# Kernel optimization log

Hardware: AMD Instinct MI355X
Metric: run time of the kernel (lower is better)

The kernel has to match this reference:

```python
import jax, jax.numpy as jnp
import numpy as np

N_NODES = 50000
N_EDGES = 800000
IN_FEATS = 128
N_HIDDEN = 128
N_CLASSES = 64


def setup_inputs() -> dict:
    key = jax.random.key(0)
    ks = jax.random.split(key, 12)
    x = jax.random.normal(ks[0], (N_NODES, IN_FEATS), dtype=jnp.float32)
    src = jax.random.randint(ks[1], (N_EDGES,), 0, N_NODES, dtype=jnp.int32)
    dst = jax.random.randint(ks[2], (N_EDGES,), 0, N_NODES, dtype=jnp.int32)
    dims = [(IN_FEATS, N_HIDDEN), (N_HIDDEN, N_HIDDEN), (N_HIDDEN, N_CLASSES)]
    inp = {"x": x, "src": src, "dst": dst}
    for i, (din, dout) in enumerate(dims):
        s = (2.0 / (din + dout)) ** 0.5  # xavier-ish init scale
        inp[f"Wself{i}"] = jax.random.normal(ks[3 + 3 * i], (din, dout), dtype=jnp.float32) * s
        inp[f"Wneigh{i}"] = jax.random.normal(ks[4 + 3 * i], (din, dout), dtype=jnp.float32) * s
        inp[f"b{i}"] = jnp.zeros((dout,), dtype=jnp.float32)
    return inp


def _sage_conv(h, src, dst, inv_deg, Wself, Wneigh, b):
    # mean aggregation over in-neighbors: gather on src, segment-sum on dst
    agg = jax.ops.segment_sum(h[src], dst, num_segments=N_NODES)  # [N, d]
    h_neigh = agg * inv_deg[:, None]
    return h @ Wself + h_neigh @ Wneigh + b


def reference(x, src, dst, Wself0, Wneigh0, b0, Wself1, Wneigh1, b1, Wself2, Wneigh2, b2):
    # in-degree (clamped to 1, matching DGL mean aggregator), shared across layers
    deg = jax.ops.segment_sum(jnp.ones((N_EDGES,), dtype=jnp.float32), dst, num_segments=N_NODES)
    inv_deg = 1.0 / jnp.maximum(deg, 1.0)
    # dropout is identity in eval mode
    h = _sage_conv(x, src, dst, inv_deg, Wself0, Wneigh0, b0)
    h = jax.nn.relu(h)
    h = _sage_conv(h, src, dst, inv_deg, Wself1, Wneigh1, b1)
    h = jax.nn.relu(h)
    h = _sage_conv(h, src, dst, inv_deg, Wself2, Wneigh2, b2)
    return h
```

## Files before the change

kernel.cpp:

```cpp
#include <hip/hip_runtime.h>

#define N_NODES 50000
#define N_EDGES 800000
#define NB_SCAN 196

typedef unsigned short ushort_t;
typedef __attribute__((ext_vector_type(8))) short  short8v;
typedef __attribute__((ext_vector_type(4))) float  float4v;
typedef __attribute__((ext_vector_type(4))) unsigned short ushort4v;
typedef __attribute__((ext_vector_type(8))) unsigned short ushort8v;

__device__ __forceinline__ ushort_t f2bf(float f) {
    unsigned u = __float_as_uint(f);
    unsigned r = 0x7fffu + ((u >> 16) & 1u);
    return (ushort_t)((u + r) >> 16);
}
__device__ __forceinline__ float bf2f(ushort_t h) {
    return __uint_as_float((unsigned)h << 16);
}

__global__ __launch_bounds__(256) void cast_zero_k(const float* __restrict__ x,
                                                   ushort_t* __restrict__ xb,
                                                   int* __restrict__ deg, int n4) {
    int i = blockIdx.x * 256 + threadIdx.x;
    if (i < n4) {
        float4 v = ((const float4*)x)[i];
        ushort4v h;
        h[0] = f2bf(v.x); h[1] = f2bf(v.y); h[2] = f2bf(v.z); h[3] = f2bf(v.w);
        ((ushort4v*)xb)[i] = h;
    }
    if (i < N_NODES) deg[i] = 0;
}

__global__ __launch_bounds__(256) void deg_count_k(const int4* __restrict__ dst4,
                                                   int* __restrict__ deg) {
    const int grp = blockIdx.x & 7;
    const int lo = grp * 6250, hi = lo + 6250;
    const int stride = (gridDim.x >> 3) * 256;
    const int n4 = N_EDGES / 4;
    for (int i = (blockIdx.x >> 3) * 256 + threadIdx.x; i < n4; i += stride) {
        int4 d = dst4[i];
        if (d.x >= lo && d.x < hi) atomicAdd(deg + d.x, 1);
        if (d.y >= lo && d.y < hi) atomicAdd(deg + d.y, 1);
        if (d.z >= lo && d.z < hi) atomicAdd(deg + d.z, 1);
        if (d.w >= lo && d.w < hi) atomicAdd(deg + d.w, 1);
    }
}

__global__ __launch_bounds__(256) void block_sum_k(const int* __restrict__ deg,
                                                   int* __restrict__ bsum, int n) {
    __shared__ int s[256];
    int t = threadIdx.x, b = blockIdx.x;
    int i = b * 256 + t;
    s[t] = (i < n) ? deg[i] : 0;
    __syncthreads();
#pragma unroll
    for (int off = 128; off > 0; off >>= 1) {
        if (t < off) s[t] += s[t + off];
        __syncthreads();
    }
    if (t == 0) bsum[b] = s[0];
}

__global__ __launch_bounds__(256) void scan_bsum_k(const int* __restrict__ bsum,
                                                   int* __restrict__ boff,
                                                   int* __restrict__ rowptr_last, int nb) {
    __shared__ int s[256];
    int t = threadIdx.x;
    int v = (t < nb) ? bsum[t] : 0;
    s[t] = v;
    __syncthreads();
#pragma unroll
    for (int off = 1; off < 256; off <<= 1) {
        int u = (t >= off) ? s[t - off] : 0;
        __syncthreads();
        s[t] += u;
        __syncthreads();
    }
    if (t < nb) boff[t] = s[t] - v;
    if (t == 255) *rowptr_last = s[255];
}

__global__ __launch_bounds__(256) void write_rowptr_k(const int* __restrict__ deg,
                                                      const int* __restrict__ boff,
                                                      int* __restrict__ rowptr,
                                                      int* __restrict__ cursor,
                                                      float* __restrict__ inv, int n) {
    __shared__ int s[256];
    int t = threadIdx.x, b = blockIdx.x;
    int i = b * 256 + t;
    int d = (i < n) ? deg[i] : 0;
    s[t] = d;
    __syncthreads();
#pragma unroll
    for (int off = 1; off < 256; off <<= 1) {
        int u = (t >= off) ? s[t - off] : 0;
        __syncthreads();
        s[t] += u;
        __syncthreads();
    }
    if (i < n) {
        int r = boff[b] + s[t] - d;
        rowptr[i] = r;
        cursor[i] = r;
        inv[i] = 1.0f / fmaxf((float)d, 1.0f);
    }
}

__global__ __launch_bounds__(256) void scatter_k(const int* __restrict__ src,
                                                 const int4* __restrict__ dst4,
                                                 int* __restrict__ cursor,
                                                 int* __restrict__ csr) {
    const int grp = blockIdx.x & 7;
    const int lo = grp * 6250, hi = lo + 6250;
    const int stride = (gridDim.x >> 3) * 256;
    const int n4 = N_EDGES / 4;
    for (int i = (blockIdx.x >> 3) * 256 + threadIdx.x; i < n4; i += stride) {
        int4 d = dst4[i];
        int e = i * 4;
        if (d.x >= lo && d.x < hi) csr[atomicAdd(cursor + d.x, 1)] = src[e + 0];
        if (d.y >= lo && d.y < hi) csr[atomicAdd(cursor + d.y, 1)] = src[e + 1];
        if (d.z >= lo && d.z < hi) csr[atomicAdd(cursor + d.z, 1)] = src[e + 2];
        if (d.w >= lo && d.w < hi) csr[atomicAdd(cursor + d.w, 1)] = src[e + 3];
    }
}

__global__ __launch_bounds__(256) void pack_all_k(const float* __restrict__ W0n, const float* __restrict__ W0s,
                                                  const float* __restrict__ W1n, const float* __restrict__ W1s,
                                                  const float* __restrict__ W2n, const float* __restrict__ W2s,
                                                  ushort_t* __restrict__ P) {
    int tid = blockIdx.x * 256 + threadIdx.x;
    const float* W; int dout; int base; int r;
    if      (tid < 2048)  { W = W0n; dout = 128; base = 0;     r = tid; }
    else if (tid < 4096)  { W = W0s; dout = 128; base = 16384; r = tid - 2048; }
    else if (tid < 6144)  { W = W1n; dout = 128; base = 32768; r = tid - 4096; }
    else if (tid < 8192)  { W = W1s; dout = 128; base = 49152; r = tid - 6144; }
    else if (tid < 9216)  { W = W2n; dout = 64;  base = 65536; r = tid - 8192; }
    else                  { W = W2s; dout = 64;  base = 73728; r = tid - 9216; }
    int lane = r & 63;
    int ks = (r >> 6) & 3;
    int nt = r >> 8;
    int col = nt * 16 + (lane & 15);
    int k0 = ks * 32 + ((lane >> 4) << 3);
    ushort_t* d = P + (size_t)base + (size_t)r * 8;
    ushort4v lo4, hi4;
#pragma unroll
    for (int j = 0; j < 4; ++j) lo4[j] = f2bf(W[(size_t)(k0 + j) * dout + col]);
#pragma unroll
    for (int j = 0; j < 4; ++j) hi4[j] = f2bf(W[(size_t)(k0 + 4 + j) * dout + col]);
    *(ushort4v*)d = lo4;
    *(ushort4v*)(d + 4) = hi4;
}

__global__ __launch_bounds__(256) void aggm_k(const ushort_t* __restrict__ h,
                                              const int* __restrict__ rowptr,
                                              const int* __restrict__ csr,
                                              const float* __restrict__ inv,
                                              ushort_t* __restrict__ m, int N) {
    int node = (blockIdx.x * 256 + threadIdx.x) >> 4;
    int c = threadIdx.x & 15;
    if (node >= N) return;
    int start = rowptr[node], end = rowptr[node + 1];

    const ushort8v* hp = (const ushort8v*)h;
    float a0[8] = {}, a1[8] = {}, a2[8] = {}, a3[8] = {};
    int j = start;
    for (; j + 3 < end; j += 4) {
        int u0 = csr[j], u1 = csr[j + 1], u2 = csr[j + 2], u3 = csr[j + 3];
        ushort8v w0 = hp[(size_t)u0 * 16 + c];
        ushort8v w1 = hp[(size_t)u1 * 16 + c];
        ushort8v w2 = hp[(size_t)u2 * 16 + c];
        ushort8v w3 = hp[(size_t)u3 * 16 + c];
#pragma unroll
        for (int k = 0; k < 8; ++k) {
            a0[k] += bf2f(w0[k]); a1[k] += bf2f(w1[k]);
            a2[k] += bf2f(w2[k]); a3[k] += bf2f(w3[k]);
        }
    }
    for (; j < end; ++j) {
        ushort8v w = hp[(size_t)csr[j] * 16 + c];
#pragma unroll
        for (int k = 0; k < 8; ++k) a0[k] += bf2f(w[k]);
    }
    float s = inv[node];
    ushort8v o;
#pragma unroll
    for (int k = 0; k < 8; ++k) o[k] = f2bf(((a0[k] + a1[k]) + (a2[k] + a3[k])) * s);
    ((ushort8v*)m)[(size_t)node * 16 + c] = o;
}

__global__ __launch_bounds__(256, 2) void fusedgemm_k(const ushort_t* __restrict__ H,
                                                      const ushort_t* __restrict__ M,
                                                      const short8v* __restrict__ Ws,
                                                      const short8v* __restrict__ Wn,
                                                      const float* __restrict__ bias,
                                                      ushort_t* __restrict__ Out, int N) {
    __shared__ ushort_t sm[2][128 * 128];
    char* sbH = (char*)sm[0];
    char* sbM = (char*)sm[1];
    const int bm = blockIdx.x * 128;
    const int t = threadIdx.x;
    const int w = t >> 6, l = t & 63;

    {
        const ushort8v* Hp = (const ushort8v*)H;
        const ushort8v* Mp = (const ushort8v*)M;
        ushort8v zeroV = {0, 0, 0, 0, 0, 0, 0, 0};
#pragma unroll
        for (int it = 0; it < 8; ++it) {
            int r = it * 16 + (t >> 4);
            int row = bm + r;
            int byte = (r * 256 + (t & 15) * 16) ^ ((r & 7) << 4);
            ushort8v vh = zeroV, vm = zeroV;
            if (row < N) {
                vh = Hp[(size_t)row * 16 + (t & 15)];
                vm = Mp[(size_t)row * 16 + (t & 15)];
            }
            *(ushort8v*)(sbH + byte) = vh;
            *(ushort8v*)(sbM + byte) = vm;
        }
    }
    __syncthreads();

    float bv[8];
#pragma unroll
    for (int nt = 0; nt < 8; ++nt) bv[nt] = bias[nt * 16 + (l & 15)];

    float4v acc[2][8] = {};
#pragma unroll
    for (int ks = 0; ks < 4; ++ks) {
        int r0 = w * 32 + (l & 15);
        int r1 = r0 + 16;
        int b0 = (r0 * 256 + ks * 64 + (l >> 4) * 16) ^ ((r0 & 7) << 4);
        int b1 = (r1 * 256 + ks * 64 + (l >> 4) * 16) ^ ((r1 & 7) << 4);
        short8v ah0 = *(const short8v*)(sbH + b0);
        short8v ah1 = *(const short8v*)(sbH + b1);
        short8v am0 = *(const short8v*)(sbM + b0);
        short8v am1 = *(const short8v*)(sbM + b1);
#pragma unroll
        for (int nt = 0; nt < 8; ++nt) {
            short8v bs = Ws[(nt * 4 + ks) * 64 + l];
            short8v bn = Wn[(nt * 4 + ks) * 64 + l];
            acc[0][nt] = __builtin_amdgcn_mfma_f32_16x16x32_bf16(ah0, bs, acc[0][nt], 0, 0, 0);
            acc[0][nt] = __builtin_amdgcn_mfma_f32_16x16x32_bf16(am0, bn, acc[0][nt], 0, 0, 0);
            acc[1][nt] = __builtin_amdgcn_mfma_f32_16x16x32_bf16(ah1, bs, acc[1][nt], 0, 0, 0);
            acc[1][nt] = __builtin_amdgcn_mfma_f32_16x16x32_bf16(am1, bn, acc[1][nt], 0, 0, 0);
        }
    }

#pragma unroll
    for (int mi = 0; mi < 2; ++mi) {
#pragma unroll
        for (int i = 0; i < 4; ++i) {
            int row = bm + w * 32 + mi * 16 + (l >> 4) * 4 + i;
            if (row < N) {
#pragma unroll
                for (int nt = 0; nt < 8; ++nt) {
                    int col = nt * 16 + (l & 15);
                    Out[(size_t)row * 128 + col] = f2bf(fmaxf(acc[mi][nt][i] + bv[nt], 0.f));
                }
            }
        }
    }
}

__global__ __launch_bounds__(256, 2) void dual64_k(const ushort_t* __restrict__ A,
                                                   const short8v* __restrict__ Wn,
                                                   const short8v* __restrict__ Ws,
                                                   const float* __restrict__ bias,
                                                   ushort_t* __restrict__ Z,
                                                   float* __restrict__ S, int N) {
    constexpr int NT = 4;
    __shared__ ushort_t Asm[128 * 128];
    char* sb = (char*)Asm;
    const int bm = blockIdx.x * 128;
    const int t = threadIdx.x;
    const int w = t >> 6, l = t & 63;

    {
        const ushort8v* Ap = (const ushort8v*)A;
        ushort8v zeroV = {0, 0, 0, 0, 0, 0, 0, 0};
#pragma unroll
        for (int it = 0; it < 8; ++it) {
            int r = it * 16 + (t >> 4);
            int row = bm + r;
            ushort8v v = zeroV;
            if (row < N) v = Ap[(size_t)row * 16 + (t & 15)];
            int byte = (r * 256 + (t & 15) * 16) ^ ((r & 7) << 4);
            *(ushort8v*)(sb + byte) = v;
        }
    }
    __syncthreads();

    float bv[NT];
#pragma unroll
    for (int nt = 0; nt < NT; ++nt) bv[nt] = bias[nt * 16 + (l & 15)];

    float4v accS[2][NT] = {}, accN[2][NT] = {};
#pragma unroll
    for (int ks = 0; ks < 4; ++ks) {
        int r0 = w * 32 + (l & 15);
        int b0 = (r0 * 256 + ks * 64 + (l >> 4) * 16) ^ ((r0 & 7) << 4);
        short8v a0 = *(const short8v*)(sb + b0);
        int r1 = r0 + 16;
        int b1 = (r1 * 256 + ks * 64 + (l >> 4) * 16) ^ ((r1 & 7) << 4);
        short8v a1 = *(const short8v*)(sb + b1);
#pragma unroll
        for (int nt = 0; nt < NT; ++nt) {
            short8v bs = Ws[(nt * 4 + ks) * 64 + l];
            short8v bn = Wn[(nt * 4 + ks) * 64 + l];
            accS[0][nt] = __builtin_amdgcn_mfma_f32_16x16x32_bf16(a0, bs, accS[0][nt], 0, 0, 0);
            accS[1][nt] = __builtin_amdgcn_mfma_f32_16x16x32_bf16(a1, bs, accS[1][nt], 0, 0, 0);
            accN[0][nt] = __builtin_amdgcn_mfma_f32_16x16x32_bf16(a0, bn, accN[0][nt], 0, 0, 0);
            accN[1][nt] = __builtin_amdgcn_mfma_f32_16x16x32_bf16(a1, bn, accN[1][nt], 0, 0, 0);
        }
    }

#pragma unroll
    for (int mi = 0; mi < 2; ++mi) {
#pragma unroll
        for (int i = 0; i < 4; ++i) {
            int row = bm + w * 32 + mi * 16 + (l >> 4) * 4 + i;
            if (row < N) {
#pragma unroll
                for (int nt = 0; nt < NT; ++nt) {
                    int col = nt * 16 + (l & 15);
                    S[(size_t)row * 64 + col] = accS[mi][nt][i] + bv[nt];
                    Z[(size_t)row * 64 + col] = f2bf(accN[mi][nt][i]);
                }
            }
        }
    }
}

__global__ __launch_bounds__(256) void agg64_k(const ushort_t* __restrict__ z,
                                               const int* __restrict__ rowptr,
                                               const int* __restrict__ csr,
                                               const float* __restrict__ inv,
                                               float* __restrict__ out, int N) {
    int node = (blockIdx.x * 256 + threadIdx.x) >> 3;
    int c = threadIdx.x & 7;
    if (node >= N) return;
    int start = rowptr[node], end = rowptr[node + 1];

    const ushort8v* zp = (const ushort8v*)z;
    float a0[8] = {}, a1[8] = {}, a2[8] = {}, a3[8] = {};
    int j = start;
    for (; j + 3 < end; j += 4) {
        int u0 = csr[j], u1 = csr[j + 1], u2 = csr[j + 2], u3 = csr[j + 3];
        ushort8v w0 = zp[(size_t)u0 * 8 + c];
        ushort8v w1 = zp[(size_t)u1 * 8 + c];
        ushort8v w2 = zp[(size_t)u2 * 8 + c];
        ushort8v w3 = zp[(size_t)u3 * 8 + c];
#pragma unroll
        for (int k = 0; k < 8; ++k) {
            a0[k] += bf2f(w0[k]); a1[k] += bf2f(w1[k]);
            a2[k] += bf2f(w2[k]); a3[k] += bf2f(w3[k]);
        }
    }
    for (; j < end; ++j) {
        ushort8v w = zp[(size_t)csr[j] * 8 + c];
#pragma unroll
        for (int k = 0; k < 8; ++k) a0[k] += bf2f(w[k]);
    }
    float s = inv[node];
    float* op = out + (size_t)node * 64 + c * 8;
    float4 o0 = *(float4*)op;
    float4 o1 = *(float4*)(op + 4);
    o0.x += ((a0[0] + a1[0]) + (a2[0] + a3[0])) * s;
    o0.y += ((a0[1] + a1[1]) + (a2[1] + a3[1])) * s;
    o0.z += ((a0[2] + a1[2]) + (a2[2] + a3[2])) * s;
    o0.w += ((a0[3] + a1[3]) + (a2[3] + a3[3])) * s;
    o1.x += ((a0[4] + a1[4]) + (a2[4] + a3[4])) * s;
    o1.y += ((a0[5] + a1[5]) + (a2[5] + a3[5])) * s;
    o1.z += ((a0[6] + a1[6]) + (a2[6] + a3[6])) * s;
    o1.w += ((a0[7] + a1[7]) + (a2[7] + a3[7])) * s;
    *(float4*)op = o0;
    *(float4*)(op + 4) = o1;
}


extern "C" void kernel_launch(void* const* d_in, const int* in_sizes, int n_in,
                              void* d_out, int out_size, void* d_ws, size_t ws_size,
                              hipStream_t stream) {
    const float* x       = (const float*)d_in[0];
    const int*   src     = (const int*)d_in[1];
    const int*   dst     = (const int*)d_in[2];
    const float* Wself0  = (const float*)d_in[3];
    const float* Wneigh0 = (const float*)d_in[4];
    const float* b0      = (const float*)d_in[5];
    const float* Wself1  = (const float*)d_in[6];
    const float* Wneigh1 = (const float*)d_in[7];
    const float* b1      = (const float*)d_in[8];
    const float* Wself2  = (const float*)d_in[9];
    const float* Wneigh2 = (const float*)d_in[10];
    const float* b2      = (const float*)d_in[11];
    float* out = (float*)d_out;

    char* ws = (char*)d_ws;
    size_t off = 0;
    auto alloc = [&](size_t bytes) -> void* {
        void* p = ws + off;
        off += (bytes + 255) & ~(size_t)255;
        return p;
    };
    int*      deg    = (int*)alloc((size_t)N_NODES * 4);
    float*    inv    = (float*)alloc((size_t)N_NODES * 4);
    int*      rowptr = (int*)alloc((size_t)(N_NODES + 1) * 4);
    int*      cursor = (int*)alloc((size_t)N_NODES * 4);
    int*      csr    = (int*)alloc((size_t)N_EDGES * 4);
    int*      bsum   = (int*)alloc((size_t)NB_SCAN * 4);
    int*      boff   = (int*)alloc((size_t)NB_SCAN * 4);
    ushort_t* packW  = (ushort_t*)alloc((size_t)81920 * 2);
    ushort_t* xb     = (ushort_t*)alloc((size_t)N_NODES * 128 * 2);
    ushort_t* mbuf   = (ushort_t*)alloc((size_t)N_NODES * 128 * 2);
    ushort_t* h1     = (ushort_t*)alloc((size_t)N_NODES * 128 * 2);
    ushort_t* h2     = (ushort_t*)alloc((size_t)N_NODES * 128 * 2);
    ushort_t* z64    = (ushort_t*)alloc((size_t)N_NODES * 64 * 2);

    dim3 b256(256);
    const int gemmBlocks  = (N_NODES + 127) / 128;
    const int aggmBlocks  = (N_NODES * 16 + 255) / 256;
    const int agg64Blocks = (N_NODES * 8 + 255) / 256;
    const int castBlocks  = (N_NODES * 32 + 255) / 256;

    cast_zero_k<<<castBlocks, b256, 0, stream>>>(x, xb, deg, N_NODES * 32);
    deg_count_k<<<1024, b256, 0, stream>>>((const int4*)dst, deg);
    block_sum_k<<<NB_SCAN, b256, 0, stream>>>(deg, bsum, N_NODES);
    scan_bsum_k<<<1, b256, 0, stream>>>(bsum, boff, rowptr + N_NODES, NB_SCAN);
    write_rowptr_k<<<NB_SCAN, b256, 0, stream>>>(deg, boff, rowptr, cursor, inv, N_NODES);
    scatter_k<<<1024, b256, 0, stream>>>(src, (const int4*)dst, cursor, csr);

    pack_all_k<<<40, b256, 0, stream>>>(Wneigh0, Wself0, Wneigh1, Wself1, Wneigh2, Wself2, packW);
    const short8v* pN0 = (const short8v*)(packW);
    const short8v* pS0 = (const short8v*)(packW + 16384);
    const short8v* pN1 = (const short8v*)(packW + 32768);
    const short8v* pS1 = (const short8v*)(packW + 49152);
    const short8v* pN2 = (const short8v*)(packW + 65536);
    const short8v* pS2 = (const short8v*)(packW + 73728);

    aggm_k<<<aggmBlocks, b256, 0, stream>>>(xb, rowptr, csr, inv, mbuf, N_NODES);
    fusedgemm_k<<<gemmBlocks, b256, 0, stream>>>(xb, mbuf, pS0, pN0, b0, h1, N_NODES);

    aggm_k<<<aggmBlocks, b256, 0, stream>>>(h1, rowptr, csr, inv, mbuf, N_NODES);
    fusedgemm_k<<<gemmBlocks, b256, 0, stream>>>(h1, mbuf, pS1, pN1, b1, h2, N_NODES);

    dual64_k<<<gemmBlocks, b256, 0, stream>>>(h2, pN2, pS2, b2, z64, out, N_NODES);
    agg64_k<<<agg64Blocks, b256, 0, stream>>>(z64, rowptr, csr, inv, out, N_NODES);
}
```

Measured before the change: 219.7 us.

## Fuse CSR scan into decoupled look-back kernel and halve GEMM tile rows

Replaces the three-kernel degree scan with one single-pass decoupled look-back scan kernel, removing two launches. Vectorizes the src loads in scatter and uses nontemporal loads for the edge arrays. Shrinks the fused GEMM and dual64 tiles from 128 to 64 rows, halving LDS per block so more blocks fit per CU and the grid has more blocks. The look-back spin-wait depends on earlier blocks being scheduled first, and smaller tiles reload the weight fragments from global memory more often per row.

After: 288.5 us. 31.3% more time.

```diff
diff --git a/kernel.cpp b/kernel.cpp
--- a/kernel.cpp
+++ b/kernel.cpp
@@ -9,6 +9,7 @@
 typedef __attribute__((ext_vector_type(4))) float  float4v;
 typedef __attribute__((ext_vector_type(4))) unsigned short ushort4v;
 typedef __attribute__((ext_vector_type(8))) unsigned short ushort8v;
+typedef __attribute__((ext_vector_type(4))) int int4v;
 
 __device__ __forceinline__ ushort_t f2bf(float f) {
     unsigned u = __float_as_uint(f);
@@ -21,7 +22,8 @@
 
 __global__ __launch_bounds__(256) void cast_zero_k(const float* __restrict__ x,
                                                    ushort_t* __restrict__ xb,
-                                                   int* __restrict__ deg, int n4) {
+                                                   int* __restrict__ deg,
+                                                   int* __restrict__ scanws, int n4) {
     int i = blockIdx.x * 256 + threadIdx.x;
     if (i < n4) {
         float4 v = ((const float4*)x)[i];
@@ -30,45 +32,37 @@
         ((ushort4v*)xb)[i] = h;
     }
     if (i < N_NODES) deg[i] = 0;
-}
-
-__global__ __launch_bounds__(256) void deg_count_k(const int4* __restrict__ dst4,
+    if (i < 3 * NB_SCAN) scanws[i] = 0;
+}
+
+__global__ __launch_bounds__(256) void deg_count_k(const int4v* __restrict__ dst4,
                                                    int* __restrict__ deg) {
     const int grp = blockIdx.x & 7;
     const int lo = grp * 6250, hi = lo + 6250;
     const int stride = (gridDim.x >> 3) * 256;
     const int n4 = N_EDGES / 4;
     for (int i = (blockIdx.x >> 3) * 256 + threadIdx.x; i < n4; i += stride) {
-        int4 d = dst4[i];
-        if (d.x >= lo && d.x < hi) atomicAdd(deg + d.x, 1);
-        if (d.y >= lo && d.y < hi) atomicAdd(deg + d.y, 1);
-        if (d.z >= lo && d.z < hi) atomicAdd(deg + d.z, 1);
-        if (d.w >= lo && d.w < hi) atomicAdd(deg + d.w, 1);
-    }
-}
-
-__global__ __launch_bounds__(256) void block_sum_k(const int* __restrict__ deg,
-                                                   int* __restrict__ bsum, int n) {
+        int4v d = __builtin_nontemporal_load(dst4 + i);
+        if (d[0] >= lo && d[0] < hi) atomicAdd(deg + d[0], 1);
+        if (d[1] >= lo && d[1] < hi) atomicAdd(deg + d[1], 1);
+        if (d[2] >= lo && d[2] < hi) atomicAdd(deg + d[2], 1);
+        if (d[3] >= lo && d[3] < hi) atomicAdd(deg + d[3], 1);
+    }
+}
+
+__global__ __launch_bounds__(256) void scan_fused_k(const int* __restrict__ deg,
+                                                    int* __restrict__ rowptr,
+                                                    int* __restrict__ cursor,
+                                                    float* __restrict__ inv,
+                                                    int* __restrict__ agg,
+                                                    int* __restrict__ prefix,
+                                                    int* __restrict__ status) {
     __shared__ int s[256];
-    int t = threadIdx.x, b = blockIdx.x;
-    int i = b * 256 + t;
-    s[t] = (i < n) ? deg[i] : 0;
-    __syncthreads();
-#pragma unroll
-    for (int off = 128; off > 0; off >>= 1) {
-        if (t < off) s[t] += s[t + off];
-        __syncthreads();
-    }
-    if (t == 0) bsum[b] = s[0];
-}
-
-__global__ __launch_bounds__(256) void scan_bsum_k(const int* __restrict__ bsum,
-                                                   int* __restrict__ boff,
-                                                   int* __restrict__ rowptr_last, int nb) {
-    __shared__ int s[256];
-    int t = threadIdx.x;
-    int v = (t < nb) ? bsum[t] : 0;
-    s[t] = v;
+    __shared__ int sExcl;
+    const int t = threadIdx.x, b = blockIdx.x;
+    const int i = b * 256 + t;
+    const int d = (i < N_NODES) ? deg[i] : 0;
+    s[t] = d;
     __syncthreads();
 #pragma unroll
     for (int off = 1; off < 256; off <<= 1) {
@@ -77,38 +71,37 @@
         s[t] += u;
         __syncthreads();
     }
-    if (t < nb) boff[t] = s[t] - v;
-    if (t == 255) *rowptr_last = s[255];
-}
-
-__global__ __launch_bounds__(256) void write_rowptr_k(const int* __restrict__ deg,
-                                                      const int* __restrict__ boff,
-                                                      int* __restrict__ rowptr,
-                                                      int* __restrict__ cursor,
-                                                      float* __restrict__ inv, int n) {
-    __shared__ int s[256];
-    int t = threadIdx.x, b = blockIdx.x;
-    int i = b * 256 + t;
-    int d = (i < n) ? deg[i] : 0;
-    s[t] = d;
+    const int total = s[255];
+    if (t == 0) {
+        __hip_atomic_store(agg + b, total, __ATOMIC_RELEASE, __HIP_MEMORY_SCOPE_AGENT);
+        __hip_atomic_store(status + b, 1, __ATOMIC_RELEASE, __HIP_MEMORY_SCOPE_AGENT);
+        int excl = 0;
+        for (int p = b - 1; p >= 0; --p) {
+            int st;
+            while ((st = __hip_atomic_load(status + p, __ATOMIC_ACQUIRE,
+                                           __HIP_MEMORY_SCOPE_AGENT)) == 0) {}
+            if (st == 2) {
+                excl += __hip_atomic_load(prefix + p, __ATOMIC_ACQUIRE, __HIP_MEMORY_SCOPE_AGENT);
+                break;
+            }
+            excl += __hip_atomic_load(agg + p, __ATOMIC_ACQUIRE, __HIP_MEMORY_SCOPE_AGENT);
+        }
+        __hip_atomic_store(prefix + b, excl + total, __ATOMIC_RELEASE, __HIP_MEMORY_SCOPE_AGENT);
+        __hip_atomic_store(status + b, 2, __ATOMIC_RELEASE, __HIP_MEMORY_SCOPE_AGENT);
+        sExcl = excl;
+        if (b == NB_SCAN - 1) rowptr[N_NODES] = excl + total;
+    }
     __syncthreads();
-#pragma unroll
-    for (int off = 1; off < 256; off <<= 1) {
-        int u = (t >= off) ? s[t - off] : 0;
-        __syncthreads();
-        s[t] += u;
-        __syncthreads();
-    }
-    if (i < n) {
-        int r = boff[b] + s[t] - d;
+    if (i < N_NODES) {
+        int r = sExcl + s[t] - d;
         rowptr[i] = r;
         cursor[i] = r;
         inv[i] = 1.0f / fmaxf((float)d, 1.0f);
     }
 }
 
-__global__ __launch_bounds__(256) void scatter_k(const int* __restrict__ src,
-                                                 const int4* __restrict__ dst4,
+__global__ __launch_bounds__(256) void scatter_k(const int4v* __restrict__ src4,
+                                                 const int4v* __restrict__ dst4,
                                                  int* __restrict__ cursor,
                                                  int* __restrict__ csr) {
     const int grp = blockIdx.x & 7;
@@ -116,12 +109,12 @@
     const int stride = (gridDim.x >> 3) * 256;
     const int n4 = N_EDGES / 4;
     for (int i = (blockIdx.x >> 3) * 256 + threadIdx.x; i < n4; i += stride) {
-        int4 d = dst4[i];
-        int e = i * 4;
-        if (d.x >= lo && d.x < hi) csr[atomicAdd(cursor + d.x, 1)] = src[e + 0];
-        if (d.y >= lo && d.y < hi) csr[atomicAdd(cursor + d.y, 1)] = src[e + 1];
-        if (d.z >= lo && d.z < hi) csr[atomicAdd(cursor + d.z, 1)] = src[e + 2];
-        if (d.w >= lo && d.w < hi) csr[atomicAdd(cursor + d.w, 1)] = src[e + 3];
+        int4v d = __builtin_nontemporal_load(dst4 + i);
+        int4v sv = __builtin_nontemporal_load(src4 + i);
+        if (d[0] >= lo && d[0] < hi) csr[atomicAdd(cursor + d[0], 1)] = sv[0];
+        if (d[1] >= lo && d[1] < hi) csr[atomicAdd(cursor + d[1], 1)] = sv[1];
+        if (d[2] >= lo && d[2] < hi) csr[atomicAdd(cursor + d[2], 1)] = sv[2];
+        if (d[3] >= lo && d[3] < hi) csr[atomicAdd(cursor + d[3], 1)] = sv[3];
     }
 }
 
@@ -189,16 +182,16 @@
     ((ushort8v*)m)[(size_t)node * 16 + c] = o;
 }
 
-__global__ __launch_bounds__(256, 2) void fusedgemm_k(const ushort_t* __restrict__ H,
+__global__ __launch_bounds__(256, 4) void fusedgemm_k(const ushort_t* __restrict__ H,
                                                       const ushort_t* __restrict__ M,
                                                       const short8v* __restrict__ Ws,
                                                       const short8v* __restrict__ Wn,
                                                       const float* __restrict__ bias,
                                                       ushort_t* __restrict__ Out, int N) {
-    __shared__ ushort_t sm[2][128 * 128];
+    __shared__ ushort_t sm[2][64 * 128];
     char* sbH = (char*)sm[0];
     char* sbM = (char*)sm[1];
-    const int bm = blockIdx.x * 128;
+    const int bm = blockIdx.x * 64;
     const int t = threadIdx.x;
     const int w = t >> 6, l = t & 63;
 
@@ -207,7 +200,7 @@
         const ushort8v* Mp = (const ushort8v*)M;
         ushort8v zeroV = {0, 0, 0, 0, 0, 0, 0, 0};
 #pragma unroll
-        for (int it = 0; it < 8; ++it) {
+        for (int it = 0; it < 4; ++it) {
             int r = it * 16 + (t >> 4);
             int row = bm + r;
             int byte = (r * 256 + (t & 15) * 16) ^ ((r & 7) << 4);
@@ -226,54 +219,45 @@
 #pragma unroll
     for (int nt = 0; nt < 8; ++nt) bv[nt] = bias[nt * 16 + (l & 15)];
 
-    float4v acc[2][8] = {};
+    float4v acc[8] = {};
 #pragma unroll
     for (int ks = 0; ks < 4; ++ks) {
-        int r0 = w * 32 + (l & 15);
-        int r1 = r0 + 16;
+        int r0 = w * 16 + (l & 15);
         int b0 = (r0 * 256 + ks * 64 + (l >> 4) * 16) ^ ((r0 & 7) << 4);
-        int b1 = (r1 * 256 + ks * 64 + (l >> 4) * 16) ^ ((r1 & 7) << 4);
-        short8v ah0 = *(const short8v*)(sbH + b0);
-        short8v ah1 = *(const short8v*)(sbH + b1);
-        short8v am0 = *(const short8v*)(sbM + b0);
-        short8v am1 = *(const short8v*)(sbM + b1);
+        short8v ah = *(const short8v*)(sbH + b0);
+        short8v am = *(const short8v*)(sbM + b0);
 #pragma unroll
         for (int nt = 0; nt < 8; ++nt) {
             short8v bs = Ws[(nt * 4 + ks) * 64 + l];
             short8v bn = Wn[(nt * 4 + ks) * 64 + l];
-            acc[0][nt] = __builtin_amdgcn_mfma_f32_16x16x32_bf16(ah0, bs, acc[0][nt], 0, 0, 0);
-            acc[0][nt] = __builtin_amdgcn_mfma_f32_16x16x32_bf16(am0, bn, acc[0][nt], 0, 0, 0);
-            acc[1][nt] = __builtin_amdgcn_mfma_f32_16x16x32_bf16(ah1, bs, acc[1][nt], 0, 0, 0);
-            acc[1][nt] = __builtin_amdgcn_mfma_f32_16x16x32_bf16(am1, bn, acc[1][nt], 0, 0, 0);
-        }
-    }
-
-#pragma unroll
-    for (int mi = 0; mi < 2; ++mi) {
-#pragma unroll
-        for (int i = 0; i < 4; ++i) {
-            int row = bm + w * 32 + mi * 16 + (l >> 4) * 4 + i;
-            if (row < N) {
-#pragma unroll
-                for (int nt = 0; nt < 8; ++nt) {
-                    int col = nt * 16 + (l & 15);
-                    Out[(size_t)row * 128 + col] = f2bf(fmaxf(acc[mi][nt][i] + bv[nt], 0.f));
-                }
+            acc[nt] = __builtin_amdgcn_mfma_f32_16x16x32_bf16(ah, bs, acc[nt], 0, 0, 0);
+            acc[nt] = __builtin_amdgcn_mfma_f32_16x16x32_bf16(am, bn, acc[nt], 0, 0, 0);
+        }
+    }
+
+#pragma unroll
+    for (int i = 0; i < 4; ++i) {
+        int row = bm + w * 16 + (l >> 4) * 4 + i;
+        if (row < N) {
+#pragma unroll
+            for (int nt = 0; nt < 8; ++nt) {
+                int col = nt * 16 + (l & 15);
+                Out[(size_t)row * 128 + col] = f2bf(fmaxf(acc[nt][i] + bv[nt], 0.f));
             }
         }
     }
 }
 
-__global__ __launch_bounds__(256, 2) void dual64_k(const ushort_t* __restrict__ A,
+__global__ __launch_bounds__(256, 4) void dual64_k(const ushort_t* __restrict__ A,
                                                    const short8v* __restrict__ Wn,
                                                    const short8v* __restrict__ Ws,
                                                    const float* __restrict__ bias,
                                                    ushort_t* __restrict__ Z,
                                                    float* __restrict__ S, int N) {
     constexpr int NT = 4;
-    __shared__ ushort_t Asm[128 * 128];
+    __shared__ ushort_t Asm[64 * 128];
     char* sb = (char*)Asm;
-    const int bm = blockIdx.x * 128;
+    const int bm = blockIdx.x * 64;
     const int t = threadIdx.x;
     const int w = t >> 6, l = t & 63;
 
@@ -281,7 +265,7 @@
         const ushort8v* Ap = (const ushort8v*)A;
         ushort8v zeroV = {0, 0, 0, 0, 0, 0, 0, 0};
 #pragma unroll
-        for (int it = 0; it < 8; ++it) {
+        for (int it = 0; it < 4; ++it) {
             int r = it * 16 + (t >> 4);
             int row = bm + r;
             ushort8v v = zeroV;
@@ -296,38 +280,30 @@
 #pragma unroll
     for (int nt = 0; nt < NT; ++nt) bv[nt] = bias[nt * 16 + (l & 15)];
 
-    float4v accS[2][NT] = {}, accN[2][NT] = {};
+    float4v accS[NT] = {}, accN[NT] = {};
 #pragma unroll
     for (int ks = 0; ks < 4; ++ks) {
-        int r0 = w * 32 + (l & 15);
+        int r0 = w * 16 + (l & 15);
         int b0 = (r0 * 256 + ks * 64 + (l >> 4) * 16) ^ ((r0 & 7) << 4);
-        short8v a0 = *(const short8v*)(sb + b0);
-        int r1 = r0 + 16;
-        int b1 = (r1 * 256 + ks * 64 + (l >> 4) * 16) ^ ((r1 & 7) << 4);
-        short8v a1 = *(const short8v*)(sb + b1);
+        short8v a = *(const short8v*)(sb + b0);
 #pragma unroll
         for (int nt = 0; nt < NT; ++nt) {
             short8v bs = Ws[(nt * 4 + ks) * 64 + l];
             short8v bn = Wn[(nt * 4 + ks) * 64 + l];
-            accS[0][nt] = __builtin_amdgcn_mfma_f32_16x16x32_bf16(a0, bs, accS[0][nt], 0, 0, 0);
-            accS[1][nt] = __builtin_amdgcn_mfma_f32_16x16x32_bf16(a1, bs, accS[1][nt], 0, 0, 0);
-            accN[0][nt] = __builtin_amdgcn_mfma_f32_16x16x32_bf16(a0, bn, accN[0][nt], 0, 0, 0);
-            accN[1][nt] = __builtin_amdgcn_mfma_f32_16x16x32_bf16(a1, bn, accN[1][nt], 0, 0, 0);
-        }
-    }
-
-#pragma unroll
-    for (int mi = 0; mi < 2; ++mi) {
-#pragma unroll
-        for (int i = 0; i < 4; ++i) {
-            int row = bm + w * 32 + mi * 16 + (l >> 4) * 4 + i;
-            if (row < N) {
-#pragma unroll
-                for (int nt = 0; nt < NT; ++nt) {
-                    int col = nt * 16 + (l & 15);
-                    S[(size_t)row * 64 + col] = accS[mi][nt][i] + bv[nt];
-                    Z[(size_t)row * 64 + col] = f2bf(accN[mi][nt][i]);
-                }
+            accS[nt] = __builtin_amdgcn_mfma_f32_16x16x32_bf16(a, bs, accS[nt], 0, 0, 0);
+            accN[nt] = __builtin_amdgcn_mfma_f32_16x16x32_bf16(a, bn, accN[nt], 0, 0, 0);
+        }
+    }
+
+#pragma unroll
+    for (int i = 0; i < 4; ++i) {
+        int row = bm + w * 16 + (l >> 4) * 4 + i;
+        if (row < N) {
+#pragma unroll
+            for (int nt = 0; nt < NT; ++nt) {
+                int col = nt * 16 + (l & 15);
+                S[(size_t)row * 64 + col] = accS[nt][i] + bv[nt];
+                Z[(size_t)row * 64 + col] = f2bf(accN[nt][i]);
             }
         }
     }
@@ -409,8 +385,7 @@
     int*      rowptr = (int*)alloc((size_t)(N_NODES + 1) * 4);
     int*      cursor = (int*)alloc((size_t)N_NODES * 4);
     int*      csr    = (int*)alloc((size_t)N_EDGES * 4);
-    int*      bsum   = (int*)alloc((size_t)NB_SCAN * 4);
-    int*      boff   = (int*)alloc((size_t)NB_SCAN * 4);
+    int*      scanws = (int*)alloc((size_t)3 * NB_SCAN * 4);
     ushort_t* packW  = (ushort_t*)alloc((size_t)81920 * 2);
     ushort_t* xb     = (ushort_t*)alloc((size_t)N_NODES * 128 * 2);
     ushort_t* mbuf   = (ushort_t*)alloc((size_t)N_NODES * 128 * 2);
@@ -419,17 +394,16 @@
     ushort_t* z64    = (ushort_t*)alloc((size_t)N_NODES * 64 * 2);
 
     dim3 b256(256);
-    const int gemmBlocks  = (N_NODES + 127) / 128;
+    const int gemmBlocks  = (N_NODES + 63) / 64;
     const int aggmBlocks  = (N_NODES * 16 + 255) / 256;
     const int agg64Blocks = (N_NODES * 8 + 255) / 256;
     const int castBlocks  = (N_NODES * 32 + 255) / 256;
 
-    cast_zero_k<<<castBlocks, b256, 0, stream>>>(x, xb, deg, N_NODES * 32);
-    deg_count_k<<<1024, b256, 0, stream>>>((const int4*)dst, deg);
-    block_sum_k<<<NB_SCAN, b256, 0, stream>>>(deg, bsum, N_NODES);
-    scan_bsum_k<<<1, b256, 0, stream>>>(bsum, boff, rowptr + N_NODES, NB_SCAN);
-    write_rowptr_k<<<NB_SCAN, b256, 0, stream>>>(deg, boff, rowptr, cursor, inv, N_NODES);
-    scatter_k<<<1024, b256, 0, stream>>>(src, (const int4*)dst, cursor, csr);
+    cast_zero_k<<<castBlocks, b256, 0, stream>>>(x, xb, deg, scanws, N_NODES * 32);
+    deg_count_k<<<1024, b256, 0, stream>>>((const int4v*)dst, deg);
+    scan_fused_k<<<NB_SCAN, b256, 0, stream>>>(deg, rowptr, cursor, inv,
+                                               scanws, scanws + NB_SCAN, scanws + 2 * NB_SCAN);
+    scatter_k<<<1024, b256, 0, stream>>>((const int4v*)src, (const int4v*)dst, cursor, csr);
 
     pack_all_k<<<40, b256, 0, stream>>>(Wneigh0, Wself0, Wneigh1, Wself1, Wneigh2, Wself2, packW);
     const short8v* pN0 = (const short8v*)(packW);
```
